# Performance work log

Hardware: AMD Instinct MI355X
Metric: run time of the kernel (lower is better)

Reference implementation:

```python
import jax, jax.numpy as jnp
import numpy as np

NUM_IMU = 72
NUM_NOISE = 12
MAX_PROP = 300
LN_EPS = 1e-5

def _softplus(x):
    return jax.nn.softplus(x)

def setup_inputs() -> dict:
    key = jax.random.key(0)
    k1, k2, k3, k4, k5 = jax.random.split(key, 5)
    d_model = 1024
    seq_len = 4096
    hidden_states = jax.random.normal(k1, (1, seq_len, d_model), dtype=jnp.float32)
    ln_gamma = jnp.ones((d_model,), dtype=jnp.float32)
    ln_beta = jnp.zeros((d_model,), dtype=jnp.float32)
    # Linear: d_model -> NUM_IMU * NUM_NOISE
    W = jax.random.normal(k2, (d_model, NUM_IMU * NUM_NOISE), dtype=jnp.float32) / np.sqrt(d_model)
    b = jax.random.normal(k3, (NUM_IMU * NUM_NOISE,), dtype=jnp.float32) * 0.01
    return {"hidden_states": hidden_states, "ln_gamma": ln_gamma, "ln_beta": ln_beta, "W": W, "b": b}

def _forward(hidden_states, ln_gamma, ln_beta, W, b):
    seq_len = hidden_states.shape[1]
    tsteps = min(MAX_PROP, seq_len)
    x = hidden_states[0]  # [seq, d_model] (squeeze batch=1)
    mu = jnp.mean(x, axis=-1, keepdims=True)
    var = jnp.mean((x - mu) ** 2, axis=-1, keepdims=True)
    xn = (x - mu) * jax.lax.rsqrt(var + LN_EPS) * ln_gamma + ln_beta
    # noise params: [seq, NUM_NOISE, NUM_IMU]
    p = (xn @ W + b).reshape(seq_len, NUM_NOISE, NUM_IMU)
    c = p[:, 4, :]
    c_theta = p[:, 5, :]
    phi = p[:, 6, :]
    phi_theta = p[:, 7, :]
    d = _softplus(p[:, 1, :])
    k = d ** 2 / 4 + _softplus(p[:, 0, :])
    d_theta = _softplus(p[:, 3, :])
    k_theta = d_theta ** 2 / 4 + _softplus(p[:, 2, :])
    acc_base = p[:, 8, :].T      # [imu, seq]
    acc_std = _softplus(p[:, 9, :]).T
    gyro_base = p[:, 10, :].T
    gyro_std = _softplus(p[:, 11, :]).T
    # vectorize over imu: move to [imu, seq, 1]
    def I(a):
        return a.T[:, :, None]
    t = jnp.arange(tsteps, dtype=jnp.float32)[None, None, :]  # [1,1,tstep]
    k_, d_, phi_, c_ = I(k), I(d), I(phi), I(c)
    kt_, dt_, pht_, ct_ = I(k_theta), I(d_theta), I(phi_theta), I(c_theta)
    omega1 = jnp.sqrt(k_ * 4 - d_ ** 2) / 2
    lin = c_ * jnp.exp(-d_ / 2 * t) * jnp.sin(t * omega1 + phi_)
    omega2 = jnp.sqrt(kt_ * 4 - dt_ ** 2) / 2
    ang = ct_ * jnp.exp(-dt_ / 2 * t) * jnp.sin(t * omega2 + pht_)
    spring = lin + ang  # [imu, seq, tstep]
    # banded scatter-add: out[s+t] += spring[:, s, t] for s+t < seq_len
    pos = jnp.arange(seq_len, dtype=jnp.int32)[:, None] + jnp.arange(tsteps, dtype=jnp.int32)[None, :]
    pos_flat = pos.reshape(-1)
    mask = pos_flat < seq_len
    pos_safe = jnp.where(mask, pos_flat, 0)
    vals = spring.reshape(NUM_IMU, -1) * mask.astype(spring.dtype)
    kinematics = jnp.zeros((NUM_IMU, seq_len), dtype=spring.dtype).at[:, pos_safe].add(vals)
    return kinematics, acc_base, acc_std, gyro_base, gyro_std

def reference(hidden_states, ln_gamma, ln_beta, W, b):
    return _forward(hidden_states, ln_gamma, ln_beta, W, b)
```

## Files before the change

kernel.cpp:

```cpp
#include <hip/hip_runtime.h>
#include <hip/hip_bf16.h>
#include <math.h>

#define SEQ 4096
#define DM  1024
#define NIMU 72
#define NNOISE 12
#define NJ (NIMU*NNOISE)
#define TSTEPS 300
#define PLANE (NIMU*SEQ)

#define A2F_SHORTS ((size_t)256 * 64 * 512)
#define BTF_SHORTS ((size_t)56 * 64 * 512)

typedef __attribute__((ext_vector_type(8))) short bf16x8;
typedef __attribute__((ext_vector_type(4))) float f32x4;

__device__ __forceinline__ float softplus_f(float x) {
    return fmaxf(x, 0.f) + log1pf(expf(-fabsf(x)));
}

__device__ __forceinline__ void split_bf16(float x, short& hi, short& lo) {
    unsigned b = __float_as_uint(x);
    unsigned h = (b + 0x7FFFu + ((b >> 16) & 1u)) >> 16;
    float hf = __uint_as_float(h << 16);
    float r = x - hf;
    unsigned b2 = __float_as_uint(r);
    unsigned l2 = (b2 + 0x7FFFu + ((b2 >> 16) & 1u)) >> 16;
    hi = (short)h;
    lo = (short)l2;
}

__global__ __launch_bounds__(256) void ln_kernel(const float* __restrict__ x,
                                                 const float* __restrict__ gamma,
                                                 const float* __restrict__ beta,
                                                 short* __restrict__ A2f) {
    const int s_tile = blockIdx.x;
    const int tid = threadIdx.x;
    const int mrow = tid >> 4;
    const int g    = tid & 15;
    const int row  = s_tile * 16 + mrow;
    const float4* xr = (const float4*)(x + (size_t)row * DM);

    float s = 0.f, sq = 0.f;
    #pragma unroll
    for (int i = 0; i < 16; ++i) {
        float4 v = xr[g + 16 * i];
        s  += v.x + v.y + v.z + v.w;
        sq += v.x*v.x + v.y*v.y + v.z*v.z + v.w*v.w;
    }
    #pragma unroll
    for (int off = 1; off < 16; off <<= 1) {
        s  += __shfl_xor(s, off);
        sq += __shfl_xor(sq, off);
    }
    const float mean = s * (1.f / DM);
    const float var  = sq * (1.f / DM) - mean * mean;
    const float rstd = rsqrtf(fmaxf(var, 0.f) + 1e-5f);

    #pragma unroll
    for (int i = 0; i < 16; ++i) {
        float4 v = xr[g + 16 * i];
        float4 gm = ((const float4*)gamma)[g + 16 * i];
        float4 bt = ((const float4*)beta)[g + 16 * i];
        float o[4];
        o[0] = (v.x - mean) * rstd * gm.x + bt.x;
        o[1] = (v.y - mean) * rstd * gm.y + bt.y;
        o[2] = (v.z - mean) * rstd * gm.z + bt.z;
        o[3] = (v.w - mean) * rstd * gm.w + bt.w;
        short4 hv, lv;
        split_bf16(o[0], hv.x, lv.x);
        split_bf16(o[1], hv.y, lv.y);
        split_bf16(o[2], hv.z, lv.z);
        split_bf16(o[3], hv.w, lv.w);
        const int ch = (g >> 3) + 2 * i;
        const size_t base = ((size_t)s_tile * 64 + ch) * 512
                          + mrow * 8 + ((g >> 1) & 3) * 128 + (g & 1) * 4;
        *(short4*)(A2f + base)             = hv;
        *(short4*)(A2f + base + 32 * 512)  = lv;
    }
}

__global__ __launch_bounds__(256) void wprep_kernel(const float* __restrict__ W,
                                                    short* __restrict__ Btf) {
    __shared__ float T[32][33];
    const int k0 = blockIdx.x * 32, j0 = blockIdx.y * 32;
    const int t = threadIdx.x;
    {
        const int r = t >> 3, c4 = (t & 7) * 4;
        float4 v = *(const float4*)(W + (size_t)(k0 + r) * NJ + j0 + c4);
        T[r][c4 + 0] = v.x; T[r][c4 + 1] = v.y; T[r][c4 + 2] = v.z; T[r][c4 + 3] = v.w;
    }
    __syncthreads();
    if (t < 128) {
        const int gq = t >> 6;
        const int l  = t & 63;
        const int n = l & 15, c = l >> 4;
        const int jt = blockIdx.y * 2 + gq;
        bf16x8 hv, lv;
        #pragma unroll
        for (int o = 0; o < 8; ++o) {
            short h, lo_;
            split_bf16(T[c * 8 + o][gq * 16 + n], h, lo_);
            hv[o] = h; lv[o] = lo_;
        }
        short* dh = Btf + ((size_t)jt * 64 + blockIdx.x) * 512 + l * 8;
        *(bf16x8*)dh = hv;
        *(bf16x8*)(dh + (size_t)32 * 512) = lv;
    }
}

__global__ __launch_bounds__(256, 1) void gemm_kernel(const short* __restrict__ A2f,
                                                      const short* __restrict__ Btf,
                                                      const float* __restrict__ bias,
                                                      float* __restrict__ pt) {
    const int l = threadIdx.x & 63, w = threadIdx.x >> 6;
    const int st0 = blockIdx.x * 8 + (w & 1) * 4;
    const int jt0 = blockIdx.y * 8 + (w >> 1) * 4;
    const short* aB = A2f + (size_t)st0 * (64 * 512) + l * 8;
    const short* bB = Btf + (size_t)jt0 * (64 * 512) + l * 8;

    f32x4 acc[4][4] = {};
    bf16x8 ah[2][4], al[2][4], bh[2][4], bl[2][4];

    auto ldstep = [&](int slot, int i) {
        #pragma unroll
        for (int t = 0; t < 4; ++t) {
            ah[slot][t] = *(const bf16x8*)(aB + ((size_t)t * 64 + i) * 512);
            al[slot][t] = *(const bf16x8*)(aB + ((size_t)t * 64 + 32 + i) * 512);
            bh[slot][t] = *(const bf16x8*)(bB + ((size_t)t * 64 + i) * 512);
            bl[slot][t] = *(const bf16x8*)(bB + ((size_t)t * 64 + 32 + i) * 512);
        }
    };

    ldstep(0, 0);
    #pragma unroll 2
    for (int i = 0; i < 32; ++i) {
        const int cur = i & 1;
        if (i + 1 < 32) ldstep(cur ^ 1, i + 1);
        #pragma unroll
        for (int mi = 0; mi < 4; ++mi)
            #pragma unroll
            for (int ni = 0; ni < 4; ++ni)
                acc[mi][ni] = __builtin_amdgcn_mfma_f32_16x16x32_bf16(
                    ah[cur][mi], bh[cur][ni], acc[mi][ni], 0, 0, 0);
        #pragma unroll
        for (int mi = 0; mi < 4; ++mi)
            #pragma unroll
            for (int ni = 0; ni < 4; ++ni)
                acc[mi][ni] = __builtin_amdgcn_mfma_f32_16x16x32_bf16(
                    ah[cur][mi], bl[cur][ni], acc[mi][ni], 0, 0, 0);
        #pragma unroll
        for (int mi = 0; mi < 4; ++mi)
            #pragma unroll
            for (int ni = 0; ni < 4; ++ni)
                acc[mi][ni] = __builtin_amdgcn_mfma_f32_16x16x32_bf16(
                    al[cur][mi], bh[cur][ni], acc[mi][ni], 0, 0, 0);
    }

    const int srow = (l >> 4) * 4;
    const int jcol = l & 15;
    #pragma unroll
    for (int ni = 0; ni < 4; ++ni) {
        const int j = (jt0 + ni) * 16 + jcol;
        if (j < NJ) {
            const float bj = bias[j];
            #pragma unroll
            for (int mi = 0; mi < 4; ++mi) {
                f32x4 v = acc[mi][ni];
                v[0] += bj; v[1] += bj; v[2] += bj; v[3] += bj;
                *(f32x4*)(pt + (size_t)j * SEQ + (st0 + mi) * 16 + srow) = v;
            }
        }
    }
}

__global__ __launch_bounds__(256) void spring_kernel(const float* __restrict__ pt,
                                                     float* __restrict__ kin) {
    const int tid  = threadIdx.x;
    const int lane = tid & 63;
    const int wid  = tid >> 6;
    const int s0   = blockIdx.x * 256;
    const int imu  = blockIdx.y;
    const int sbase = s0 + (wid << 6);
    const int s    = sbase + lane;

    const int base = imu * SEQ + s;
    const float p0  = pt[(size_t)0 * PLANE + base];
    const float p1  = pt[(size_t)1 * PLANE + base];
    const float p2  = pt[(size_t)2 * PLANE + base];
    const float p3  = pt[(size_t)3 * PLANE + base];
    const float c1  = pt[(size_t)4 * PLANE + base];
    const float c2  = pt[(size_t)5 * PLANE + base];
    const float ph1 = pt[(size_t)6 * PLANE + base];
    const float ph2 = pt[(size_t)7 * PLANE + base];

    float dd = softplus_f(p1);
    float kk = dd * dd * 0.25f + softplus_f(p0);
    float om1 = 0.5f * sqrtf(fmaxf(4.f * kk - dd * dd, 0.f));
    float dt = softplus_f(p3);
    float kt = dt * dt * 0.25f + softplus_f(p2);
    float om2 = 0.5f * sqrtf(fmaxf(4.f * kt - dt * dt, 0.f));
    float e1 = expf(-0.5f * dd), e2 = expf(-0.5f * dt);
    float sn, cs;
    sincosf(om1, &sn, &cs); const float mr1 = e1 * cs, mi1 = e1 * sn;
    sincosf(om2, &sn, &cs); const float mr2 = e2 * cs, mi2 = e2 * sn;
    sincosf(ph1, &sn, &cs); float im1 = c1 * sn, re1 = c1 * cs;
    sincosf(ph2, &sn, &cs); float im2 = c2 * sn, re2 = c2 * cs;

    float A[6];
    #pragma unroll
    for (int r = 0; r < 6; ++r) A[r] = 0.f;

    const bool full = (sbase + 64 + TSTEPS <= SEQ);

    if (full) {
        #pragma unroll
        for (int tq = 0; tq < 5; ++tq) {
            const int trmax = (tq == 4) ? 44 : 64;
            for (int tr0 = 0; tr0 < trmax; tr0 += 4) {
                float v[4], u[4];
                #pragma unroll
                for (int i = 0; i < 4; ++i) {
                    v[i] = im1 + im2;
                    float r1 = fmaf(re1, mr1, -im1 * mi1);
                    im1 = fmaf(re1, mi1, im1 * mr1);
                    re1 = r1;
                    float r2 = fmaf(re2, mr2, -im2 * mi2);
                    im2 = fmaf(re2, mi2, im2 * mr2);
                    re2 = r2;
                }
                #pragma unroll
                for (int i = 0; i < 4; ++i)
                    u[i] = __shfl(v[i], (lane - (tr0 + i)) & 63);
                #pragma unroll
                for (int i = 0; i < 4; ++i) {
                    const int tr = tr0 + i;
                    A[tq]     += (lane >= tr) ? u[i] : 0.f;
                    A[tq + 1] += (lane <  tr) ? u[i] : 0.f;
                }
            }
        }
    } else {
        const int tmax_wave = min(TSTEPS, SEQ - sbase);
        const int tmax_lane = SEQ - s;
        #pragma unroll
        for (int tq = 0; tq < 5; ++tq) {
            const int trmax = min(64, tmax_wave - tq * 64);
            for (int tr = 0; tr < trmax; ++tr) {
                const int t = tq * 64 + tr;
                float val = (t < tmax_lane) ? (im1 + im2) : 0.f;
                float u = __shfl(val, (lane - tr) & 63);
                A[tq]     += (lane >= tr) ? u : 0.f;
                A[tq + 1] += (lane <  tr) ? u : 0.f;
                float r1 = fmaf(re1, mr1, -im1 * mi1);
                im1 = fmaf(re1, mi1, im1 * mr1);
                re1 = r1;
                float r2 = fmaf(re2, mr2, -im2 * mi2);
                im2 = fmaf(re2, mi2, im2 * mr2);
                re2 = r2;
            }
            if (trmax < 64) break;
        }
    }

    #pragma unroll
    for (int r = 0; r < 6; ++r) {
        int pos = sbase + 64 * r + lane;
        if (pos < SEQ) {
            __hip_atomic_fetch_add(&kin[(size_t)imu * SEQ + pos], A[r],
                                   __ATOMIC_RELAXED, __HIP_MEMORY_SCOPE_AGENT);
        }
    }
}

__global__ __launch_bounds__(256) void tail_kernel(const float* __restrict__ pt,
                                                   float* __restrict__ out) {
    int idx = blockIdx.x * 256 + threadIdx.x;
    if (idx >= 4 * PLANE) return;
    float v = pt[(size_t)8 * PLANE + idx];
    int q = idx / PLANE;
    if (q & 1) v = softplus_f(v);
    out[(size_t)PLANE + idx] = v;
}

extern "C" void kernel_launch(void* const* d_in, const int* in_sizes, int n_in,
                              void* d_out, int out_size, void* d_ws, size_t ws_size,
                              hipStream_t stream) {
    const float* hs    = (const float*)d_in[0];
    const float* gamma = (const float*)d_in[1];
    const float* beta  = (const float*)d_in[2];
    const float* W     = (const float*)d_in[3];
    const float* b     = (const float*)d_in[4];
    float* out = (float*)d_out;

    short* A2f = (short*)d_ws;
    short* Btf = A2f + A2F_SHORTS;
    float* pt  = (float*)(Btf + BTF_SHORTS);

    hipMemsetAsync(out, 0, (size_t)PLANE * sizeof(float), stream);

    ln_kernel<<<SEQ / 16, 256, 0, stream>>>(hs, gamma, beta, A2f);
    wprep_kernel<<<dim3(DM / 32, NJ / 32), 256, 0, stream>>>(W, Btf);
    gemm_kernel<<<dim3(SEQ / 128, 7), 256, 0, stream>>>(A2f, Btf, b, pt);
    spring_kernel<<<dim3(SEQ / 256, NIMU), 256, 0, stream>>>(pt, out);
    tail_kernel<<<(4 * PLANE + 255) / 256, 256, 0, stream>>>(pt, out);
}
```

Baseline: 169.2 us.

## Split spring time steps across two grid halves and pack damped rotations as float2

The spring kernel's 300-step recurrence is split into two halves along a new grid z dimension. The second half jumps its starting phasor ahead by R^152 using exponentiation by squaring. The two complex rotations are packed into float2 vectors so they can use packed FP32 math. This doubles the number of blocks and halves the serial chain per thread, aiming to hide latency better. The cost is extra atomics on overlapping output ranges and some rounding drift from the power computation.

```diff
diff --git a/kernel.cpp b/kernel.cpp
--- a/kernel.cpp
+++ b/kernel.cpp
@@ -15,6 +15,7 @@
 
 typedef __attribute__((ext_vector_type(8))) short bf16x8;
 typedef __attribute__((ext_vector_type(4))) float f32x4;
+typedef __attribute__((ext_vector_type(2))) float f32x2;
 
 __device__ __forceinline__ float softplus_f(float x) {
     return fmaxf(x, 0.f) + log1pf(expf(-fabsf(x)));
@@ -182,6 +183,9 @@
     const int wid  = tid >> 6;
     const int s0   = blockIdx.x * 256;
     const int imu  = blockIdx.y;
+    const int th   = blockIdx.z;
+    const int tbeg = th ? 152 : 0;
+    const int tlen = th ? 148 : 152;
     const int sbase = s0 + (wid << 6);
     const int s    = sbase + lane;
 
@@ -202,33 +206,54 @@
     float kt = dt * dt * 0.25f + softplus_f(p2);
     float om2 = 0.5f * sqrtf(fmaxf(4.f * kt - dt * dt, 0.f));
     float e1 = expf(-0.5f * dd), e2 = expf(-0.5f * dt);
-    float sn, cs;
-    sincosf(om1, &sn, &cs); const float mr1 = e1 * cs, mi1 = e1 * sn;
-    sincosf(om2, &sn, &cs); const float mr2 = e2 * cs, mi2 = e2 * sn;
-    sincosf(ph1, &sn, &cs); float im1 = c1 * sn, re1 = c1 * cs;
-    sincosf(ph2, &sn, &cs); float im2 = c2 * sn, re2 = c2 * cs;
-
-    float A[6];
-    #pragma unroll
-    for (int r = 0; r < 6; ++r) A[r] = 0.f;
-
-    const bool full = (sbase + 64 + TSTEPS <= SEQ);
+    float sn, cs, sn2, cs2;
+    sincosf(om1, &sn, &cs);
+    sincosf(om2, &sn2, &cs2);
+    f32x2 Rr = {e1 * cs, e2 * cs2};
+    f32x2 Ri = {e1 * sn, e2 * sn2};
+    sincosf(ph1, &sn, &cs);
+    sincosf(ph2, &sn2, &cs2);
+    f32x2 zr = {c1 * cs, c2 * cs2};
+    f32x2 zi = {c1 * sn, c2 * sn2};
+
+    if (th) {
+        f32x2 prr = Rr, pri = Ri;
+        f32x2 qr = {1.f, 1.f}, qi = {0.f, 0.f};
+        int e = 152;
+        while (e) {
+            if (e & 1) {
+                f32x2 nr = qr * prr - qi * pri;
+                qi = qr * pri + qi * prr;
+                qr = nr;
+            }
+            f32x2 nr = prr * prr - pri * pri;
+            pri = 2.f * prr * pri;
+            prr = nr;
+            e >>= 1;
+        }
+        f32x2 nr = zr * qr - zi * qi;
+        zi = zr * qi + zi * qr;
+        zr = nr;
+    }
+
+    float A[4];
+    #pragma unroll
+    for (int r = 0; r < 4; ++r) A[r] = 0.f;
+
+    const bool full = (sbase + 63 + tbeg + tlen - 1) < SEQ;
 
     if (full) {
         #pragma unroll
-        for (int tq = 0; tq < 5; ++tq) {
-            const int trmax = (tq == 4) ? 44 : 64;
+        for (int tq = 0; tq < 3; ++tq) {
+            const int trmax = (tq == 2) ? (tlen - 128) : 64;
             for (int tr0 = 0; tr0 < trmax; tr0 += 4) {
                 float v[4], u[4];
                 #pragma unroll
                 for (int i = 0; i < 4; ++i) {
-                    v[i] = im1 + im2;
-                    float r1 = fmaf(re1, mr1, -im1 * mi1);
-                    im1 = fmaf(re1, mi1, im1 * mr1);
-                    re1 = r1;
-                    float r2 = fmaf(re2, mr2, -im2 * mi2);
-                    im2 = fmaf(re2, mi2, im2 * mr2);
-                    re2 = r2;
+                    v[i] = zi.x + zi.y;
+                    f32x2 nr = zr * Rr - zi * Ri;
+                    zi = zr * Ri + zi * Rr;
+                    zr = nr;
                 }
                 #pragma unroll
                 for (int i = 0; i < 4; ++i)
@@ -242,34 +267,33 @@
             }
         }
     } else {
-        const int tmax_wave = min(TSTEPS, SEQ - sbase);
-        const int tmax_lane = SEQ - s;
-        #pragma unroll
-        for (int tq = 0; tq < 5; ++tq) {
-            const int trmax = min(64, tmax_wave - tq * 64);
+        const int tmax_lane = SEQ - s - tbeg;
+        #pragma unroll
+        for (int tq = 0; tq < 3; ++tq) {
+            const int trmax = (tq == 2) ? (tlen - 128) : 64;
             for (int tr = 0; tr < trmax; ++tr) {
-                const int t = tq * 64 + tr;
-                float val = (t < tmax_lane) ? (im1 + im2) : 0.f;
+                const int t2 = tq * 64 + tr;
+                float val = (t2 < tmax_lane) ? (zi.x + zi.y) : 0.f;
                 float u = __shfl(val, (lane - tr) & 63);
                 A[tq]     += (lane >= tr) ? u : 0.f;
                 A[tq + 1] += (lane <  tr) ? u : 0.f;
-                float r1 = fmaf(re1, mr1, -im1 * mi1);
-                im1 = fmaf(re1, mi1, im1 * mr1);
-                re1 = r1;
-                float r2 = fmaf(re2, mr2, -im2 * mi2);
-                im2 = fmaf(re2, mi2, im2 * mr2);
-                re2 = r2;
-            }
-            if (trmax < 64) break;
-        }
-    }
-
-    #pragma unroll
-    for (int r = 0; r < 6; ++r) {
-        int pos = sbase + 64 * r + lane;
-        if (pos < SEQ) {
-            __hip_atomic_fetch_add(&kin[(size_t)imu * SEQ + pos], A[r],
-                                   __ATOMIC_RELAXED, __HIP_MEMORY_SCOPE_AGENT);
+                f32x2 nr = zr * Rr - zi * Ri;
+                zi = zr * Ri + zi * Rr;
+                zr = nr;
+            }
+        }
+    }
+
+    const int pbase = sbase + tbeg;
+    #pragma unroll
+    for (int r = 0; r < 4; ++r) {
+        const int idx = r * 64 + lane;
+        if (idx < tlen + 63) {
+            const int pos = pbase + idx;
+            if (pos < SEQ) {
+                __hip_atomic_fetch_add(&kin[(size_t)imu * SEQ + pos], A[r],
+                                       __ATOMIC_RELAXED, __HIP_MEMORY_SCOPE_AGENT);
+            }
         }
     }
 }
@@ -303,6 +327,6 @@
     ln_kernel<<<SEQ / 16, 256, 0, stream>>>(hs, gamma, beta, A2f);
     wprep_kernel<<<dim3(DM / 32, NJ / 32), 256, 0, stream>>>(W, Btf);
     gemm_kernel<<<dim3(SEQ / 128, 7), 256, 0, stream>>>(A2f, Btf, b, pt);
-    spring_kernel<<<dim3(SEQ / 256, NIMU), 256, 0, stream>>>(pt, out);
+    spring_kernel<<<dim3(SEQ / 256, NIMU, 2), 256, 0, stream>>>(pt, out);
     tail_kernel<<<(4 * PLANE + 255) / 256, 256, 0, stream>>>(pt, out);
 }
```

Measured after the change: 159.8 us. 5.5% less time.
